# Kernel optimization log

Hardware: AMD Instinct MI355X
Metric: run time of the kernel (lower is better)

Reference implementation:

```python
import jax, jax.numpy as jnp
import numpy as np

N, E, H, R, A = 100000, 1600000, 128, 500, 16  # nodes, edges, hidden, reservoir, actions
LN_EPS = 1e-5

def setup_inputs() -> dict:
    key = jax.random.key(0)
    ks = jax.random.split(key, 8)
    return {
        "node_feats": jax.random.normal(ks[0], (N, 2), jnp.float32),
        "edge_index": jax.random.randint(ks[1], (2, E), 0, N, dtype=jnp.int32),
        "esn_state": jax.random.normal(ks[2], (1, R), jnp.float32),
        "gcn_w": jax.random.normal(ks[3], (2, H), jnp.float32) * 0.5,
        "gcn_b": jnp.zeros((H,), jnp.float32),
        "ln_w": jnp.ones((H,), jnp.float32),
        "ln_b": jnp.zeros((H,), jnp.float32),
        "fc1_w": jax.random.normal(ks[4], (H + R, H), jnp.float32) * 0.04,
        "fc1_b": jnp.zeros((H,), jnp.float32),
        "fc2_w": jax.random.normal(ks[5], (H, A), jnp.float32) * 0.08,
        "fc2_b": jnp.zeros((A,), jnp.float32),
    }

def reference(node_feats, edge_index, esn_state, gcn_w, gcn_b, ln_w, ln_b,
              fc1_w, fc1_b, fc2_w, fc2_b):
    src, dst = edge_index[0], edge_index[1]
    n = node_feats.shape[0]
    # GCNConv: linear transform, then symmetric-normalized aggregation with self-loops
    h = node_feats @ gcn_w  # [N, H]
    deg = jax.ops.segment_sum(jnp.ones_like(src, dtype=h.dtype), dst, num_segments=n) + 1.0
    dis = jax.lax.rsqrt(deg)  # deg >= 1 due to self-loops
    norm = dis[src] * dis[dst]  # [E]
    agg = jax.ops.segment_sum(h[src] * norm[:, None], dst, num_segments=n)  # [N, H]
    x = agg + h * (dis * dis)[:, None] + gcn_b  # self-loop term + bias
    x = jax.nn.relu(x)
    # PyG LayerNorm, mode='graph', batch=None: normalize over all nodes & channels
    x = x - x.mean()
    x = x / (jnp.sqrt(x.var()) + LN_EPS)
    x = x * ln_w + ln_b
    pooled = x.sum(axis=0, keepdims=True)  # global_add_pool, single graph -> [1, H]
    z = jnp.concatenate([pooled, esn_state], axis=1)  # [1, H+R]
    z = jax.nn.relu(z @ fc1_w + fc1_b)
    logits = z @ fc2_w + fc2_b  # [1, A]
    return jax.nn.log_softmax(logits, axis=1)
```

## Files before the change

kernel.cpp:

```cpp
#include <hip/hip_runtime.h>
#include <math.h>

#define NN 100000
#define EE 1600000
#define HH 128
#define RR 500
#define AA 16
#define LN_EPS 1e-5f

#define BSH 8
#define NPB 256
#define NB 391
#define MAXPB 4608
#define EPW 6252
#define SCT 512
#define NWG_SC 256
#define NZW 64

__global__ __launch_bounds__(256) void k_init_esn(unsigned int* __restrict__ zero_region,
                                                  const float* __restrict__ esn,
                                                  const float* __restrict__ fc1_w,
                                                  float* __restrict__ zpart) {
    const int w = blockIdx.x, t = threadIdx.x;
    if (w == 0) {
        for (int j = t; j < 512 + HH + 1; j += 256) zero_region[j] = 0u;
        return;
    }
    const int sl = w - 1;
    const int k0 = sl * 8;
    const int k1 = min(k0 + 8, RR);
    if (t < HH) {
        float acc = 0.f;
        for (int k = k0; k < k1; ++k)
            acc = fmaf(esn[k], fc1_w[(size_t)(HH + k) * HH + t], acc);
        zpart[(size_t)sl * HH + t] = acc;
    }
}

__global__ __launch_bounds__(SCT) void k_scatter(const int* __restrict__ src,
                                                 const int* __restrict__ dst,
                                                 unsigned int* __restrict__ gctr,
                                                 unsigned int* __restrict__ payload) {
    __shared__ unsigned int hist[512], rank[512], hbase[512];
    const int t = threadIdx.x;
    hist[t] = 0u; rank[t] = 0u; hbase[t] = 0u;
    __syncthreads();
    const int e0 = blockIdx.x * EPW;
    const int ecnt = max(0, min(EPW, EE - e0));
    const int nv = ecnt >> 2;
    const int4* d4 = reinterpret_cast<const int4*>(dst + e0);
    const int4* s4 = reinterpret_cast<const int4*>(src + e0);

    for (int k = t; k < nv; k += SCT) {
        int4 d = d4[k];
        atomicAdd(&hist[((unsigned)d.x) >> BSH], 1u);
        atomicAdd(&hist[((unsigned)d.y) >> BSH], 1u);
        atomicAdd(&hist[((unsigned)d.z) >> BSH], 1u);
        atomicAdd(&hist[((unsigned)d.w) >> BSH], 1u);
    }
    __syncthreads();

    if (t < NB && hist[t] > 0u) hbase[t] = atomicAdd(&gctr[t], hist[t]);
    __syncthreads();

    for (int k = t; k < nv; k += SCT) {
        int4 d = d4[k];
        int4 s = s4[k];
        #define EMIT(SS, DD) { \
            unsigned int dd = (unsigned)(DD), ss = (unsigned)(SS); \
            unsigned int b = dd >> BSH; \
            unsigned int r = atomicAdd(&rank[b], 1u); \
            unsigned int slot = hbase[b] + r; \
            if (slot < MAXPB) payload[(size_t)b * MAXPB + slot] = (ss << BSH) | (dd & (NPB - 1)); }
        EMIT(s.x, d.x) EMIT(s.y, d.y) EMIT(s.z, d.z) EMIT(s.w, d.w)
        #undef EMIT
    }
}

__global__ __launch_bounds__(1024) void k_bdeg_g(const unsigned int* __restrict__ gctr,
                                                 const unsigned int* __restrict__ payload,
                                                 const float* __restrict__ nf,
                                                 float* __restrict__ rsv, float* __restrict__ g) {
    __shared__ unsigned int hist[NPB];
    const int b = blockIdx.x, t = threadIdx.x;
    if (t < NPB) hist[t] = 0u;
    __syncthreads();
    const unsigned int cnt = min(gctr[b], (unsigned int)MAXPB);
    const unsigned int* pl = payload + (size_t)b * MAXPB;
    const uint4* pl4 = reinterpret_cast<const uint4*>(pl);
    const unsigned int nv = cnt >> 2;
    for (unsigned int k = t; k < nv; k += 1024) {
        uint4 p = pl4[k];
        atomicAdd(&hist[p.x & (NPB - 1)], 1u);
        atomicAdd(&hist[p.y & (NPB - 1)], 1u);
        atomicAdd(&hist[p.z & (NPB - 1)], 1u);
        atomicAdd(&hist[p.w & (NPB - 1)], 1u);
    }
    for (unsigned int k = (nv << 2) + t; k < cnt; k += 1024)
        atomicAdd(&hist[pl[k] & (NPB - 1)], 1u);
    __syncthreads();
    if (t < NPB) {
        int node = (b << BSH) + t;
        if (node < NN) {
            float df = 1.0f + (float)hist[t];
            float rs = rsqrtf(df);
            rsv[node] = rs;
            float2 f = *reinterpret_cast<const float2*>(&nf[2 * node]);
            float2 gv; gv.x = rs * f.x; gv.y = rs * f.y;
            *reinterpret_cast<float2*>(&g[2 * node]) = gv;
        }
    }
}

__global__ __launch_bounds__(1024) void k_bagg_node(const unsigned int* __restrict__ gctr,
        const unsigned int* __restrict__ payload,
        const float* __restrict__ g, const float* __restrict__ rsv,
        const float* __restrict__ gcn_w, const float* __restrict__ gcn_b,
        float* __restrict__ S, float* __restrict__ T2) {
    __shared__ float agg[NPB * 2];
    __shared__ float shSf[HH];
    __shared__ float shw[16];
    const int b = blockIdx.x, t = threadIdx.x;
    if (t < NPB * 2) agg[t] = 0.f;
    if (t < HH) shSf[t] = 0.f;
    __syncthreads();
    const unsigned int cnt = min(gctr[b], (unsigned int)MAXPB);
    const unsigned int* pl = payload + (size_t)b * MAXPB;
    const uint4* pl4 = reinterpret_cast<const uint4*>(pl);
    const unsigned int nv = cnt >> 2;
    for (unsigned int k = t; k < nv; k += 1024) {
        uint4 p = pl4[k];
        #define ACC(P) { \
            unsigned int s = (P) >> BSH, dl = (P) & (NPB - 1); \
            float2 gv = *reinterpret_cast<const float2*>(&g[2 * s]); \
            atomicAdd(&agg[dl],       gv.x); \
            atomicAdd(&agg[NPB + dl], gv.y); }
        ACC(p.x) ACC(p.y) ACC(p.z) ACC(p.w)
        #undef ACC
    }
    for (unsigned int k = (nv << 2) + t; k < cnt; k += 1024) {
        unsigned int p = pl[k];
        unsigned int s = p >> BSH, dl = p & (NPB - 1);
        float2 gv = *reinterpret_cast<const float2*>(&g[2 * s]);
        atomicAdd(&agg[dl],       gv.x);
        atomicAdd(&agg[NPB + dl], gv.y);
    }
    __syncthreads();

    const int nvalid = min(NPB, NN - (b << BSH));
    if (t < nvalid) {
        int node = (b << BSH) + t;
        float rs = rsv[node];
        float2 gv = *reinterpret_cast<const float2*>(&g[2 * node]);
        agg[t]       = rs * (agg[t]       + gv.x);
        agg[NPB + t] = rs * (agg[NPB + t] + gv.y);
    }
    __syncthreads();

    const int ch = t & (HH - 1), slot = t >> 7;
    const float w0 = gcn_w[ch], w1 = gcn_w[HH + ch], bb = gcn_b[ch];
    float accS = 0.f, accT2 = 0.f;
    for (int j = slot; j < nvalid; j += 8) {
        float x = fmaf(agg[j], w0, fmaf(agg[NPB + j], w1, bb));
        float r = fmaxf(x, 0.f);
        accS  += r;
        accT2 += r * r;
    }
    atomicAdd(&shSf[ch], accS);
    float v = accT2;
    for (int o = 32; o; o >>= 1) v += __shfl_down(v, o, 64);
    if ((t & 63) == 0) shw[t >> 6] = v;
    __syncthreads();
    if (t < HH) atomicAdd(&S[t], shSf[t]);
    if (t == 0) {
        float s2 = 0.f;
        #pragma unroll
        for (int w = 0; w < 16; ++w) s2 += shw[w];
        atomicAdd(T2, s2);
    }
}

__global__ __launch_bounds__(1024) void k_final2(const float* __restrict__ S,
                        const float* __restrict__ T2ptr,
                        const float* __restrict__ zpart,
                        const float* __restrict__ ln_w, const float* __restrict__ ln_b,
                        const float* __restrict__ fc1_w, const float* __restrict__ fc1_b,
                        const float* __restrict__ fc2_w, const float* __restrict__ fc2_b,
                        float* __restrict__ out) {
    const int t = threadIdx.x;
    const int ch = t & (HH - 1), sl = t >> 7;
    __shared__ float psum[8][HH];
    __shared__ float sh_pooled[HH], sh_z[HH], sh_logits[AA];
    __shared__ float shred[2];

    if (t < HH) {
        float s = S[t];
        sh_pooled[t] = s;
        float vv = s;
        for (int o = 32; o; o >>= 1) vv += __shfl_down(vv, o, 64);
        if ((t & 63) == 0) shred[t >> 6] = vv;
    }
    __syncthreads();

    const float T1 = shred[0] + shred[1];
    const float T2 = *T2ptr;
    const float cnt = (float)NN * (float)HH;
    const float mean = T1 / cnt;
    const float var  = T2 / cnt - mean * mean;
    const float denom = sqrtf(var) + LN_EPS;
    if (t < HH)
        sh_pooled[t] = ln_w[t] * (sh_pooled[t] - (float)NN * mean) / denom + (float)NN * ln_b[t];
    __syncthreads();

    float acc = 0.f;
    for (int k = sl * 16; k < sl * 16 + 16; ++k)
        acc = fmaf(sh_pooled[k], fc1_w[(size_t)k * HH + ch], acc);
    for (int w = sl * 8; w < sl * 8 + 8; ++w)
        acc += zpart[(size_t)w * HH + ch];
    psum[sl][ch] = acc;
    __syncthreads();
    if (t < HH) {
        float a = fc1_b[t];
        #pragma unroll
        for (int k = 0; k < 8; ++k) a += psum[k][t];
        sh_z[t] = fmaxf(a, 0.f);
    }
    __syncthreads();

    if (t < AA) {
        float l = fc2_b[t];
        for (int j = 0; j < HH; ++j)
            l = fmaf(sh_z[j], fc2_w[j * AA + t], l);
        sh_logits[t] = l;
    }
    __syncthreads();

    if (t == 0) {
        float m = sh_logits[0];
        for (int a = 1; a < AA; ++a) m = fmaxf(m, sh_logits[a]);
        float sum = 0.f;
        for (int a = 0; a < AA; ++a) sum += expf(sh_logits[a] - m);
        float lse = m + logf(sum);
        for (int a = 0; a < AA; ++a) out[a] = sh_logits[a] - lse;
    }
}


__global__ void k_initf(unsigned int* __restrict__ p, int n) {
    int i = blockIdx.x * blockDim.x + threadIdx.x;
    int stride = gridDim.x * blockDim.x;
    for (int j = i; j < n; j += stride) p[j] = 0u;
}

__global__ void k_deg1(const int* __restrict__ dst, int* __restrict__ deg, int e) {
    int i = blockIdx.x * blockDim.x + threadIdx.x;
    if (i < e) atomicAdd(&deg[dst[i]], 1);
}

__global__ void k_g1(const int* __restrict__ deg, const float* __restrict__ nf,
                     float* __restrict__ degf, float* __restrict__ g, int n) {
    int i = blockIdx.x * blockDim.x + threadIdx.x;
    if (i < n) {
        float df = (float)(1 + deg[i]);
        degf[i] = df;
        float rs = rsqrtf(df);
        float2 f = *reinterpret_cast<const float2*>(&nf[2 * i]);
        float2 gv; gv.x = rs * f.x; gv.y = rs * f.y;
        *reinterpret_cast<float2*>(&g[2 * i]) = gv;
    }
}

__global__ void k_edge1(const int* __restrict__ src, const int* __restrict__ dst,
                        const float* __restrict__ g, float* __restrict__ B, int e) {
    int i = blockIdx.x * blockDim.x + threadIdx.x;
    if (i < e) {
        int s = src[i], d = dst[i];
        float2 gv = *reinterpret_cast<const float2*>(&g[2 * s]);
        atomicAdd(&B[2 * d],     gv.x);
        atomicAdd(&B[2 * d + 1], gv.y);
    }
}

__global__ void k_node(const float* __restrict__ nf, const float* __restrict__ degf,
                       const float* __restrict__ B,
                       const float* __restrict__ gcn_w, const float* __restrict__ gcn_b,
                       float* __restrict__ S, float* __restrict__ T2, int n) {
    const int ch   = threadIdx.x & (HH - 1);
    const int slot = threadIdx.x >> 7;
    const float w0 = gcn_w[ch];
    const float w1 = gcn_w[HH + ch];
    const float b  = gcn_b[ch];
    float accS = 0.f, accT2 = 0.f;
    for (int i = blockIdx.x * 2 + slot; i < n; i += gridDim.x * 2) {
        float df   = degf[i];
        float invd = 1.0f / df;
        float rs   = rsqrtf(df);
        float2 bv = *reinterpret_cast<const float2*>(&B[2 * i]);
        float2 f  = *reinterpret_cast<const float2*>(&nf[2 * i]);
        float b0 = rs * bv.x + f.x * invd;
        float b1 = rs * bv.y + f.y * invd;
        float xv = fmaf(b0, w0, fmaf(b1, w1, b));
        float r  = fmaxf(xv, 0.f);
        accS  += r;
        accT2 += r * r;
    }
    __shared__ float shS[HH];
    if (slot == 1) shS[ch] = accS;
    __syncthreads();
    if (slot == 0) atomicAdd(&S[ch], accS + shS[ch]);
    float v = accT2;
    for (int o = 32; o; o >>= 1) v += __shfl_down(v, o, 64);
    __shared__ float shw[4];
    if ((threadIdx.x & 63) == 0) shw[threadIdx.x >> 6] = v;
    __syncthreads();
    if (threadIdx.x == 0) atomicAdd(T2, shw[0] + shw[1] + shw[2] + shw[3]);
}

__global__ void k_final(const float* __restrict__ S, const float* __restrict__ T2ptr,
                        const float* __restrict__ esn,
                        const float* __restrict__ ln_w, const float* __restrict__ ln_b,
                        const float* __restrict__ fc1_w, const float* __restrict__ fc1_b,
                        const float* __restrict__ fc2_w, const float* __restrict__ fc2_b,
                        float* __restrict__ out) {
    const int t = threadIdx.x;
    __shared__ float sh_pooled[HH];
    __shared__ float sh_z[HH];
    __shared__ float sh_logits[AA];
    __shared__ float shred[2];

    float s = S[t];
    float v = s;
    for (int o = 32; o; o >>= 1) v += __shfl_down(v, o, 64);
    if ((t & 63) == 0) shred[t >> 6] = v;
    __syncthreads();
    const float T1 = shred[0] + shred[1];
    const float T2 = *T2ptr;
    const float cnt = (float)NN * (float)HH;
    const float mean = T1 / cnt;
    const float var  = T2 / cnt - mean * mean;
    const float denom = sqrtf(var) + LN_EPS;
    sh_pooled[t] = ln_w[t] * (s - (float)NN * mean) / denom + (float)NN * ln_b[t];
    __syncthreads();

    float acc = fc1_b[t];
    for (int k = 0; k < HH; ++k)
        acc = fmaf(sh_pooled[k], fc1_w[k * HH + t], acc);
    for (int k = 0; k < RR; ++k)
        acc = fmaf(esn[k], fc1_w[(HH + k) * HH + t], acc);
    sh_z[t] = fmaxf(acc, 0.f);
    __syncthreads();

    if (t < AA) {
        float l = fc2_b[t];
        for (int j = 0; j < HH; ++j)
            l = fmaf(sh_z[j], fc2_w[j * AA + t], l);
        sh_logits[t] = l;
    }
    __syncthreads();

    if (t == 0) {
        float m = sh_logits[0];
        for (int a = 1; a < AA; ++a) m = fmaxf(m, sh_logits[a]);
        float sum = 0.f;
        for (int a = 0; a < AA; ++a) sum += expf(sh_logits[a] - m);
        float lse = m + logf(sum);
        for (int a = 0; a < AA; ++a) out[a] = sh_logits[a] - lse;
    }
}

extern "C" void kernel_launch(void* const* d_in, const int* in_sizes, int n_in,
                              void* d_out, int out_size, void* d_ws, size_t ws_size,
                              hipStream_t stream) {
    const float* nf     = (const float*)d_in[0];
    const int*   ei     = (const int*)d_in[1];
    const float* esn    = (const float*)d_in[2];
    const float* gcn_w  = (const float*)d_in[3];
    const float* gcn_b  = (const float*)d_in[4];
    const float* ln_w   = (const float*)d_in[5];
    const float* ln_b   = (const float*)d_in[6];
    const float* fc1_w  = (const float*)d_in[7];
    const float* fc1_b  = (const float*)d_in[8];
    const float* fc2_w  = (const float*)d_in[9];
    const float* fc2_b  = (const float*)d_in[10];
    float* out = (float*)d_out;
    float* ws  = (float*)d_ws;

    const size_t OFF_S       = 512;
    const size_t OFF_T2      = OFF_S + HH;
    const size_t OFF_ZPART   = ((OFF_T2 + 1 + 3) & ~(size_t)3);
    const size_t OFF_PAYLOAD = OFF_ZPART + (size_t)NZW * HH;
    const size_t OFF_RSV     = OFF_PAYLOAD + (size_t)NB * MAXPB;
    const size_t OFF_G       = OFF_RSV + NN;
    const size_t NEED_BKT    = (OFF_G + 2 * (size_t)NN) * 4;

    if (ws_size >= NEED_BKT) {
        unsigned int* gctr    = (unsigned int*)ws;
        float*        S       = ws + OFF_S;
        float*        T2      = ws + OFF_T2;
        float*        zpart   = ws + OFF_ZPART;
        unsigned int* payload = (unsigned int*)ws + OFF_PAYLOAD;
        float*        rsv     = ws + OFF_RSV;
        float*        g       = ws + OFF_G;

        hipLaunchKernelGGL(k_init_esn,  dim3(NZW + 1), dim3(256),  0, stream, (unsigned int*)ws, esn, fc1_w, zpart);
        hipLaunchKernelGGL(k_scatter,   dim3(NWG_SC),  dim3(SCT),  0, stream, ei, ei + EE, gctr, payload);
        hipLaunchKernelGGL(k_bdeg_g,    dim3(NB),      dim3(1024), 0, stream, gctr, payload, nf, rsv, g);
        hipLaunchKernelGGL(k_bagg_node, dim3(NB),      dim3(1024), 0, stream, gctr, payload, g, rsv, gcn_w, gcn_b, S, T2);
        hipLaunchKernelGGL(k_final2,    dim3(1),       dim3(1024), 0, stream,
                           S, T2, zpart, ln_w, ln_b, fc1_w, fc1_b, fc2_w, fc2_b, out);
    } else {
        int*   deg  = (int*)ws;
        float* B    = ws + NN;
        float* S    = ws + 3 * (size_t)NN;
        float* T2   = ws + 3 * (size_t)NN + 128;
        float* degf = ws + 3 * (size_t)NN + 130;
        float* g    = ws + 4 * (size_t)NN + 130;
        const int eb = (EE + 255) / 256;
        const int nb = (NN + 255) / 256;
        hipLaunchKernelGGL(k_initf, dim3(2048), dim3(256), 0, stream, (unsigned int*)ws, 3 * NN + 129);
        hipLaunchKernelGGL(k_deg1,  dim3(eb),   dim3(256), 0, stream, ei + EE, deg, EE);
        hipLaunchKernelGGL(k_g1,    dim3(nb),   dim3(256), 0, stream, deg, nf, degf, g, NN);
        hipLaunchKernelGGL(k_edge1, dim3(eb),   dim3(256), 0, stream, ei, ei + EE, g, B, EE);
        hipLaunchKernelGGL(k_node,  dim3(512),  dim3(256), 0, stream, nf, degf, B, gcn_w, gcn_b, S, T2, NN);
        hipLaunchKernelGGL(k_final, dim3(1),    dim3(128), 0, stream,
                           S, T2, esn, ln_w, ln_b, fc1_w, fc1_b, fc2_w, fc2_b, out);
    }
}
```

Before: 67.45 us.

## Fuse five-kernel GCN pipeline into one cooperative persistent kernel with grid syncs

Replaces the five separate launches (init/esn, scatter, degree, aggregate, final) with a single cooperative kernel of 256 workgroups × 1024 threads that separates the stages with grid.sync. Shared memory is unioned across stages, and the bucket stages loop over the 391 buckets with a stride of 256 workgroups. The goal is to remove per-launch overhead and inter-kernel gaps. In exchange, the 391 buckets no longer spread evenly over the 256 workgroups, the scatter stage now runs 1024 threads per block instead of 512, and grid-wide barriers add their own cost.

Result: slower. 187.6 us (+178.0%).

```diff
diff --git a/kernel.cpp b/kernel.cpp
--- a/kernel.cpp
+++ b/kernel.cpp
@@ -1,5 +1,8 @@
 #include <hip/hip_runtime.h>
+#include <hip/hip_cooperative_groups.h>
 #include <math.h>
+
+namespace cg = cooperative_groups;
 
 #define NN 100000
 #define EE 1600000
@@ -12,236 +15,229 @@
 #define NPB 256
 #define NB 391
 #define MAXPB 4608
+#define NWG 256
+#define TPB 1024
 #define EPW 6252
-#define SCT 512
-#define NWG_SC 256
 #define NZW 64
 
-__global__ __launch_bounds__(256) void k_init_esn(unsigned int* __restrict__ zero_region,
-                                                  const float* __restrict__ esn,
-                                                  const float* __restrict__ fc1_w,
-                                                  float* __restrict__ zpart) {
-    const int w = blockIdx.x, t = threadIdx.x;
-    if (w == 0) {
-        for (int j = t; j < 512 + HH + 1; j += 256) zero_region[j] = 0u;
-        return;
-    }
-    const int sl = w - 1;
-    const int k0 = sl * 8;
-    const int k1 = min(k0 + 8, RR);
-    if (t < HH) {
+
+__global__ __launch_bounds__(TPB) void k_fused(
+    const float* __restrict__ nf, const int* __restrict__ srcp, const int* __restrict__ dstp,
+    const float* __restrict__ esn,
+    const float* __restrict__ gcn_w, const float* __restrict__ gcn_b,
+    const float* __restrict__ ln_w, const float* __restrict__ ln_b,
+    const float* __restrict__ fc1_w, const float* __restrict__ fc1_b,
+    const float* __restrict__ fc2_w, const float* __restrict__ fc2_b,
+    unsigned int* __restrict__ gctr, float* __restrict__ S, float* __restrict__ T2,
+    float* __restrict__ zpart, unsigned int* __restrict__ payload,
+    float* __restrict__ rsv, float* __restrict__ g, float* __restrict__ out)
+{
+    cg::grid_group grid = cg::this_grid();
+    const int wg = blockIdx.x, t = threadIdx.x;
+
+    __shared__ union {
+        struct { unsigned int hist[512], rank[512], hbase[512]; } sc;
+        struct { unsigned int hist[NPB]; } bd;
+        struct { float agg[NPB * 2]; float shSf[HH]; float shw[16]; } ba;
+        struct { float psum[8][HH]; float pooled[HH]; float z[HH];
+                 float logits[AA]; float red[2]; } fin;
+    } u;
+
+    if (wg == 0) {
+        for (int j = t; j < 641; j += TPB) gctr[j] = 0u;
+    } else if (wg <= NZW) {
+        const int sl = wg - 1;
+        const int k0 = sl * 8, k1 = min(k0 + 8, RR);
+        if (t < HH) {
+            float acc = 0.f;
+            for (int k = k0; k < k1; ++k)
+                acc = fmaf(esn[k], fc1_w[(size_t)(HH + k) * HH + t], acc);
+            zpart[(size_t)sl * HH + t] = acc;
+        }
+    }
+    grid.sync();
+
+    {
+        if (t < 512) { u.sc.hist[t] = 0u; u.sc.rank[t] = 0u; u.sc.hbase[t] = 0u; }
+        __syncthreads();
+        const int e0 = wg * EPW;
+        const int ecnt = max(0, min(EPW, EE - e0));
+        const int nv = ecnt >> 2;
+        const int4* d4 = reinterpret_cast<const int4*>(dstp + e0);
+        const int4* s4 = reinterpret_cast<const int4*>(srcp + e0);
+
+        for (int k = t; k < nv; k += TPB) {
+            int4 d = d4[k];
+            atomicAdd(&u.sc.hist[((unsigned)d.x) >> BSH], 1u);
+            atomicAdd(&u.sc.hist[((unsigned)d.y) >> BSH], 1u);
+            atomicAdd(&u.sc.hist[((unsigned)d.z) >> BSH], 1u);
+            atomicAdd(&u.sc.hist[((unsigned)d.w) >> BSH], 1u);
+        }
+        __syncthreads();
+        if (t < NB && u.sc.hist[t] > 0u) u.sc.hbase[t] = atomicAdd(&gctr[t], u.sc.hist[t]);
+        __syncthreads();
+        for (int k = t; k < nv; k += TPB) {
+            int4 d = d4[k];
+            int4 s = s4[k];
+            #define EMIT(SS, DD) { \
+                unsigned int dd = (unsigned)(DD), ss = (unsigned)(SS); \
+                unsigned int b = dd >> BSH; \
+                unsigned int r = atomicAdd(&u.sc.rank[b], 1u); \
+                unsigned int slot = u.sc.hbase[b] + r; \
+                if (slot < MAXPB) payload[(size_t)b * MAXPB + slot] = (ss << BSH) | (dd & (NPB - 1)); }
+            EMIT(s.x, d.x) EMIT(s.y, d.y) EMIT(s.z, d.z) EMIT(s.w, d.w)
+            #undef EMIT
+        }
+    }
+    grid.sync();
+
+    for (int b = wg; b < NB; b += NWG) {
+        if (t < NPB) u.bd.hist[t] = 0u;
+        __syncthreads();
+        const unsigned int cnt = min(gctr[b], (unsigned int)MAXPB);
+        const unsigned int* pl = payload + (size_t)b * MAXPB;
+        const uint4* pl4 = reinterpret_cast<const uint4*>(pl);
+        const unsigned int nv2 = cnt >> 2;
+        for (unsigned int k = t; k < nv2; k += TPB) {
+            uint4 p = pl4[k];
+            atomicAdd(&u.bd.hist[p.x & (NPB - 1)], 1u);
+            atomicAdd(&u.bd.hist[p.y & (NPB - 1)], 1u);
+            atomicAdd(&u.bd.hist[p.z & (NPB - 1)], 1u);
+            atomicAdd(&u.bd.hist[p.w & (NPB - 1)], 1u);
+        }
+        for (unsigned int k = (nv2 << 2) + t; k < cnt; k += TPB)
+            atomicAdd(&u.bd.hist[pl[k] & (NPB - 1)], 1u);
+        __syncthreads();
+        if (t < NPB) {
+            int node = (b << BSH) + t;
+            if (node < NN) {
+                float df = 1.0f + (float)u.bd.hist[t];
+                float rs = rsqrtf(df);
+                rsv[node] = rs;
+                float2 f = *reinterpret_cast<const float2*>(&nf[2 * node]);
+                float2 gv; gv.x = rs * f.x; gv.y = rs * f.y;
+                *reinterpret_cast<float2*>(&g[2 * node]) = gv;
+            }
+        }
+        __syncthreads();
+    }
+    grid.sync();
+
+    {
+        const int ch = t & (HH - 1), slot = t >> 7;
+        const float w0 = gcn_w[ch], w1 = gcn_w[HH + ch], bb = gcn_b[ch];
+        float accS = 0.f, accT2 = 0.f;
+        if (t < HH) u.ba.shSf[t] = 0.f;
+        for (int b = wg; b < NB; b += NWG) {
+            if (t < NPB * 2) u.ba.agg[t] = 0.f;
+            __syncthreads();
+            const unsigned int cnt = min(gctr[b], (unsigned int)MAXPB);
+            const unsigned int* pl = payload + (size_t)b * MAXPB;
+            const uint4* pl4 = reinterpret_cast<const uint4*>(pl);
+            const unsigned int nv2 = cnt >> 2;
+            for (unsigned int k = t; k < nv2; k += TPB) {
+                uint4 p = pl4[k];
+                #define ACC(P) { \
+                    unsigned int s = (P) >> BSH, dl = (P) & (NPB - 1); \
+                    float2 gv = *reinterpret_cast<const float2*>(&g[2 * s]); \
+                    atomicAdd(&u.ba.agg[dl],       gv.x); \
+                    atomicAdd(&u.ba.agg[NPB + dl], gv.y); }
+                ACC(p.x) ACC(p.y) ACC(p.z) ACC(p.w)
+                #undef ACC
+            }
+            for (unsigned int k = (nv2 << 2) + t; k < cnt; k += TPB) {
+                unsigned int p = pl[k];
+                unsigned int s = p >> BSH, dl = p & (NPB - 1);
+                float2 gv = *reinterpret_cast<const float2*>(&g[2 * s]);
+                atomicAdd(&u.ba.agg[dl],       gv.x);
+                atomicAdd(&u.ba.agg[NPB + dl], gv.y);
+            }
+            __syncthreads();
+
+            const int nvalid = min(NPB, NN - (b << BSH));
+            if (t < nvalid) {
+                int node = (b << BSH) + t;
+                float rs = rsv[node];
+                float2 gv = *reinterpret_cast<const float2*>(&g[2 * node]);
+                u.ba.agg[t]       = rs * (u.ba.agg[t]       + gv.x);
+                u.ba.agg[NPB + t] = rs * (u.ba.agg[NPB + t] + gv.y);
+            }
+            __syncthreads();
+
+            for (int j = slot; j < nvalid; j += 8) {
+                float x = fmaf(u.ba.agg[j], w0, fmaf(u.ba.agg[NPB + j], w1, bb));
+                float r = fmaxf(x, 0.f);
+                accS  += r;
+                accT2 += r * r;
+            }
+            __syncthreads();
+        }
+        atomicAdd(&u.ba.shSf[ch], accS);
+        float v = accT2;
+        for (int o = 32; o; o >>= 1) v += __shfl_down(v, o, 64);
+        if ((t & 63) == 0) u.ba.shw[t >> 6] = v;
+        __syncthreads();
+        if (t < HH) atomicAdd(&S[t], u.ba.shSf[t]);
+        if (t == 0) {
+            float s2 = 0.f;
+            #pragma unroll
+            for (int w = 0; w < 16; ++w) s2 += u.ba.shw[w];
+            atomicAdd(T2, s2);
+        }
+    }
+    grid.sync();
+
+    if (wg == 0) {
+        const int ch = t & (HH - 1), sl = t >> 7;
+        if (t < HH) {
+            float s = S[t];
+            u.fin.pooled[t] = s;
+            float vv = s;
+            for (int o = 32; o; o >>= 1) vv += __shfl_down(vv, o, 64);
+            if ((t & 63) == 0) u.fin.red[t >> 6] = vv;
+        }
+        __syncthreads();
+        const float T1 = u.fin.red[0] + u.fin.red[1];
+        const float T2v = *T2;
+        const float cntf = (float)NN * (float)HH;
+        const float mean = T1 / cntf;
+        const float var  = T2v / cntf - mean * mean;
+        const float denom = sqrtf(var) + LN_EPS;
+        if (t < HH)
+            u.fin.pooled[t] = ln_w[t] * (u.fin.pooled[t] - (float)NN * mean) / denom + (float)NN * ln_b[t];
+        __syncthreads();
+
         float acc = 0.f;
-        for (int k = k0; k < k1; ++k)
-            acc = fmaf(esn[k], fc1_w[(size_t)(HH + k) * HH + t], acc);
-        zpart[(size_t)sl * HH + t] = acc;
-    }
-}
-
-__global__ __launch_bounds__(SCT) void k_scatter(const int* __restrict__ src,
-                                                 const int* __restrict__ dst,
-                                                 unsigned int* __restrict__ gctr,
-                                                 unsigned int* __restrict__ payload) {
-    __shared__ unsigned int hist[512], rank[512], hbase[512];
-    const int t = threadIdx.x;
-    hist[t] = 0u; rank[t] = 0u; hbase[t] = 0u;
-    __syncthreads();
-    const int e0 = blockIdx.x * EPW;
-    const int ecnt = max(0, min(EPW, EE - e0));
-    const int nv = ecnt >> 2;
-    const int4* d4 = reinterpret_cast<const int4*>(dst + e0);
-    const int4* s4 = reinterpret_cast<const int4*>(src + e0);
-
-    for (int k = t; k < nv; k += SCT) {
-        int4 d = d4[k];
-        atomicAdd(&hist[((unsigned)d.x) >> BSH], 1u);
-        atomicAdd(&hist[((unsigned)d.y) >> BSH], 1u);
-        atomicAdd(&hist[((unsigned)d.z) >> BSH], 1u);
-        atomicAdd(&hist[((unsigned)d.w) >> BSH], 1u);
-    }
-    __syncthreads();
-
-    if (t < NB && hist[t] > 0u) hbase[t] = atomicAdd(&gctr[t], hist[t]);
-    __syncthreads();
-
-    for (int k = t; k < nv; k += SCT) {
-        int4 d = d4[k];
-        int4 s = s4[k];
-        #define EMIT(SS, DD) { \
-            unsigned int dd = (unsigned)(DD), ss = (unsigned)(SS); \
-            unsigned int b = dd >> BSH; \
-            unsigned int r = atomicAdd(&rank[b], 1u); \
-            unsigned int slot = hbase[b] + r; \
-            if (slot < MAXPB) payload[(size_t)b * MAXPB + slot] = (ss << BSH) | (dd & (NPB - 1)); }
-        EMIT(s.x, d.x) EMIT(s.y, d.y) EMIT(s.z, d.z) EMIT(s.w, d.w)
-        #undef EMIT
-    }
-}
-
-__global__ __launch_bounds__(1024) void k_bdeg_g(const unsigned int* __restrict__ gctr,
-                                                 const unsigned int* __restrict__ payload,
-                                                 const float* __restrict__ nf,
-                                                 float* __restrict__ rsv, float* __restrict__ g) {
-    __shared__ unsigned int hist[NPB];
-    const int b = blockIdx.x, t = threadIdx.x;
-    if (t < NPB) hist[t] = 0u;
-    __syncthreads();
-    const unsigned int cnt = min(gctr[b], (unsigned int)MAXPB);
-    const unsigned int* pl = payload + (size_t)b * MAXPB;
-    const uint4* pl4 = reinterpret_cast<const uint4*>(pl);
-    const unsigned int nv = cnt >> 2;
-    for (unsigned int k = t; k < nv; k += 1024) {
-        uint4 p = pl4[k];
-        atomicAdd(&hist[p.x & (NPB - 1)], 1u);
-        atomicAdd(&hist[p.y & (NPB - 1)], 1u);
-        atomicAdd(&hist[p.z & (NPB - 1)], 1u);
-        atomicAdd(&hist[p.w & (NPB - 1)], 1u);
-    }
-    for (unsigned int k = (nv << 2) + t; k < cnt; k += 1024)
-        atomicAdd(&hist[pl[k] & (NPB - 1)], 1u);
-    __syncthreads();
-    if (t < NPB) {
-        int node = (b << BSH) + t;
-        if (node < NN) {
-            float df = 1.0f + (float)hist[t];
-            float rs = rsqrtf(df);
-            rsv[node] = rs;
-            float2 f = *reinterpret_cast<const float2*>(&nf[2 * node]);
-            float2 gv; gv.x = rs * f.x; gv.y = rs * f.y;
-            *reinterpret_cast<float2*>(&g[2 * node]) = gv;
-        }
-    }
-}
-
-__global__ __launch_bounds__(1024) void k_bagg_node(const unsigned int* __restrict__ gctr,
-        const unsigned int* __restrict__ payload,
-        const float* __restrict__ g, const float* __restrict__ rsv,
-        const float* __restrict__ gcn_w, const float* __restrict__ gcn_b,
-        float* __restrict__ S, float* __restrict__ T2) {
-    __shared__ float agg[NPB * 2];
-    __shared__ float shSf[HH];
-    __shared__ float shw[16];
-    const int b = blockIdx.x, t = threadIdx.x;
-    if (t < NPB * 2) agg[t] = 0.f;
-    if (t < HH) shSf[t] = 0.f;
-    __syncthreads();
-    const unsigned int cnt = min(gctr[b], (unsigned int)MAXPB);
-    const unsigned int* pl = payload + (size_t)b * MAXPB;
-    const uint4* pl4 = reinterpret_cast<const uint4*>(pl);
-    const unsigned int nv = cnt >> 2;
-    for (unsigned int k = t; k < nv; k += 1024) {
-        uint4 p = pl4[k];
-        #define ACC(P) { \
-            unsigned int s = (P) >> BSH, dl = (P) & (NPB - 1); \
-            float2 gv = *reinterpret_cast<const float2*>(&g[2 * s]); \
-            atomicAdd(&agg[dl],       gv.x); \
-            atomicAdd(&agg[NPB + dl], gv.y); }
-        ACC(p.x) ACC(p.y) ACC(p.z) ACC(p.w)
-        #undef ACC
-    }
-    for (unsigned int k = (nv << 2) + t; k < cnt; k += 1024) {
-        unsigned int p = pl[k];
-        unsigned int s = p >> BSH, dl = p & (NPB - 1);
-        float2 gv = *reinterpret_cast<const float2*>(&g[2 * s]);
-        atomicAdd(&agg[dl],       gv.x);
-        atomicAdd(&agg[NPB + dl], gv.y);
-    }
-    __syncthreads();
-
-    const int nvalid = min(NPB, NN - (b << BSH));
-    if (t < nvalid) {
-        int node = (b << BSH) + t;
-        float rs = rsv[node];
-        float2 gv = *reinterpret_cast<const float2*>(&g[2 * node]);
-        agg[t]       = rs * (agg[t]       + gv.x);
-        agg[NPB + t] = rs * (agg[NPB + t] + gv.y);
-    }
-    __syncthreads();
-
-    const int ch = t & (HH - 1), slot = t >> 7;
-    const float w0 = gcn_w[ch], w1 = gcn_w[HH + ch], bb = gcn_b[ch];
-    float accS = 0.f, accT2 = 0.f;
-    for (int j = slot; j < nvalid; j += 8) {
-        float x = fmaf(agg[j], w0, fmaf(agg[NPB + j], w1, bb));
-        float r = fmaxf(x, 0.f);
-        accS  += r;
-        accT2 += r * r;
-    }
-    atomicAdd(&shSf[ch], accS);
-    float v = accT2;
-    for (int o = 32; o; o >>= 1) v += __shfl_down(v, o, 64);
-    if ((t & 63) == 0) shw[t >> 6] = v;
-    __syncthreads();
-    if (t < HH) atomicAdd(&S[t], shSf[t]);
-    if (t == 0) {
-        float s2 = 0.f;
-        #pragma unroll
-        for (int w = 0; w < 16; ++w) s2 += shw[w];
-        atomicAdd(T2, s2);
-    }
-}
-
-__global__ __launch_bounds__(1024) void k_final2(const float* __restrict__ S,
-                        const float* __restrict__ T2ptr,
-                        const float* __restrict__ zpart,
-                        const float* __restrict__ ln_w, const float* __restrict__ ln_b,
-                        const float* __restrict__ fc1_w, const float* __restrict__ fc1_b,
-                        const float* __restrict__ fc2_w, const float* __restrict__ fc2_b,
-                        float* __restrict__ out) {
-    const int t = threadIdx.x;
-    const int ch = t & (HH - 1), sl = t >> 7;
-    __shared__ float psum[8][HH];
-    __shared__ float sh_pooled[HH], sh_z[HH], sh_logits[AA];
-    __shared__ float shred[2];
-
-    if (t < HH) {
-        float s = S[t];
-        sh_pooled[t] = s;
-        float vv = s;
-        for (int o = 32; o; o >>= 1) vv += __shfl_down(vv, o, 64);
-        if ((t & 63) == 0) shred[t >> 6] = vv;
-    }
-    __syncthreads();
-
-    const float T1 = shred[0] + shred[1];
-    const float T2 = *T2ptr;
-    const float cnt = (float)NN * (float)HH;
-    const float mean = T1 / cnt;
-    const float var  = T2 / cnt - mean * mean;
-    const float denom = sqrtf(var) + LN_EPS;
-    if (t < HH)
-        sh_pooled[t] = ln_w[t] * (sh_pooled[t] - (float)NN * mean) / denom + (float)NN * ln_b[t];
-    __syncthreads();
-
-    float acc = 0.f;
-    for (int k = sl * 16; k < sl * 16 + 16; ++k)
-        acc = fmaf(sh_pooled[k], fc1_w[(size_t)k * HH + ch], acc);
-    for (int w = sl * 8; w < sl * 8 + 8; ++w)
-        acc += zpart[(size_t)w * HH + ch];
-    psum[sl][ch] = acc;
-    __syncthreads();
-    if (t < HH) {
-        float a = fc1_b[t];
-        #pragma unroll
-        for (int k = 0; k < 8; ++k) a += psum[k][t];
-        sh_z[t] = fmaxf(a, 0.f);
-    }
-    __syncthreads();
-
-    if (t < AA) {
-        float l = fc2_b[t];
-        for (int j = 0; j < HH; ++j)
-            l = fmaf(sh_z[j], fc2_w[j * AA + t], l);
-        sh_logits[t] = l;
-    }
-    __syncthreads();
-
-    if (t == 0) {
-        float m = sh_logits[0];
-        for (int a = 1; a < AA; ++a) m = fmaxf(m, sh_logits[a]);
-        float sum = 0.f;
-        for (int a = 0; a < AA; ++a) sum += expf(sh_logits[a] - m);
-        float lse = m + logf(sum);
-        for (int a = 0; a < AA; ++a) out[a] = sh_logits[a] - lse;
+        for (int k = sl * 16; k < sl * 16 + 16; ++k)
+            acc = fmaf(u.fin.pooled[k], fc1_w[(size_t)k * HH + ch], acc);
+        for (int w = sl * 8; w < sl * 8 + 8; ++w)
+            acc += zpart[(size_t)w * HH + ch];
+        u.fin.psum[sl][ch] = acc;
+        __syncthreads();
+        if (t < HH) {
+            float a = fc1_b[t];
+            #pragma unroll
+            for (int k = 0; k < 8; ++k) a += u.fin.psum[k][t];
+            u.fin.z[t] = fmaxf(a, 0.f);
+        }
+        __syncthreads();
+
+        if (t < AA) {
+            float l = fc2_b[t];
+            for (int j = 0; j < HH; ++j)
+                l = fmaf(u.fin.z[j], fc2_w[j * AA + t], l);
+            u.fin.logits[t] = l;
+        }
+        __syncthreads();
+
+        if (t == 0) {
+            float m = u.fin.logits[0];
+            for (int a = 1; a < AA; ++a) m = fmaxf(m, u.fin.logits[a]);
+            float sum = 0.f;
+            for (int a = 0; a < AA; ++a) sum += expf(u.fin.logits[a] - m);
+            float lse = m + logf(sum);
+            for (int a = 0; a < AA; ++a) out[a] = u.fin.logits[a] - lse;
+        }
     }
 }
 
@@ -402,12 +398,17 @@
         float*        rsv     = ws + OFF_RSV;
         float*        g       = ws + OFF_G;
 
-        hipLaunchKernelGGL(k_init_esn,  dim3(NZW + 1), dim3(256),  0, stream, (unsigned int*)ws, esn, fc1_w, zpart);
-        hipLaunchKernelGGL(k_scatter,   dim3(NWG_SC),  dim3(SCT),  0, stream, ei, ei + EE, gctr, payload);
-        hipLaunchKernelGGL(k_bdeg_g,    dim3(NB),      dim3(1024), 0, stream, gctr, payload, nf, rsv, g);
-        hipLaunchKernelGGL(k_bagg_node, dim3(NB),      dim3(1024), 0, stream, gctr, payload, g, rsv, gcn_w, gcn_b, S, T2);
-        hipLaunchKernelGGL(k_final2,    dim3(1),       dim3(1024), 0, stream,
-                           S, T2, zpart, ln_w, ln_b, fc1_w, fc1_b, fc2_w, fc2_b, out);
+        const int* srcp = ei;
+        const int* dstp = ei + EE;
+        void* args[] = {
+            (void*)&nf, (void*)&srcp, (void*)&dstp, (void*)&esn,
+            (void*)&gcn_w, (void*)&gcn_b, (void*)&ln_w, (void*)&ln_b,
+            (void*)&fc1_w, (void*)&fc1_b, (void*)&fc2_w, (void*)&fc2_b,
+            (void*)&gctr, (void*)&S, (void*)&T2, (void*)&zpart,
+            (void*)&payload, (void*)&rsv, (void*)&g, (void*)&out
+        };
+        hipLaunchCooperativeKernel((const void*)k_fused, dim3(NWG), dim3(TPB),
+                                   args, 0, stream);
     } else {
         int*   deg  = (int*)ws;
         float* B    = ws + NN;
```
